# Performance work log

Hardware: AMD Instinct MI355X
Metric: run time of the kernel (lower is better)

## Reference

```python
import jax, jax.numpy as jnp
import numpy as np

B, T, C, F = 32, 512, 256, 512


def setup_inputs() -> dict:
    key = jax.random.key(0)
    k1, k2, k3 = jax.random.split(key, 3)
    x = jax.random.normal(k1, (B, T, F), dtype=jnp.float32)
    # glorot-uniform-ish learned params
    context = jax.random.normal(k2, (C, F), dtype=jnp.float32) * (1.0 / np.sqrt(F))
    W = jax.random.normal(k3, (2 * F, 1), dtype=jnp.float32) * (1.0 / np.sqrt(2 * F))
    b = jnp.zeros((1,), dtype=jnp.float32)
    return {"x": x, "context": context, "W": W, "b": b}


def reference(x, context, W, b):
    # Original: concat(tile(x)->[B,T,C,F], tile(context)->[B,T,C,F]) @ W[2F,1] + b.
    # Decompose W = [W_x; W_c] so the [B,T,C,2F] tensor is never materialized.
    f = x.shape[-1]
    s_x = x @ W[:f] + b            # [B, T, 1]
    s_c = context @ W[f:]          # [C, 1]
    scores = s_x[:, :, None, :] + s_c[None, None, :, :]  # [B, T, C, 1]
    # Keras Activation('softmax') acts on the LAST axis (size 1) -> all ones;
    # computed literally for faithfulness.
    att = jax.nn.softmax(scores, axis=-1)[..., 0]        # [B, T, C]
    # multiply by expanded_x and sum over time axis (axis=1)
    out = jnp.einsum('btc,btf->bcf', att, x)             # [B, C, F]
    return out
```

## Files before the change

kernel.cpp:

```cpp
#include <hip/hip_runtime.h>


#define BB 32
#define TT 512
#define CC 256
#define FF 512
#define F4 (FF / 4)
#define FC 8

__device__ __forceinline__ void acc4(float4& a, const float4& v) {
    a.x += v.x; a.y += v.y; a.z += v.z; a.w += v.w;
}

__global__ __launch_bounds__(512) void colsum_bcast(const float4* __restrict__ x4,
                                                    float4* __restrict__ out4) {
    __shared__ float4 lds[32][16];

    const int tid = threadIdx.x;
    const int f4l = tid & 15;
    const int g   = tid >> 4;
    const int b   = blockIdx.x >> 3;
    const int fc  = blockIdx.x & 7;

    const float4* xp = x4 + (size_t)b * TT * F4 + fc * 16 + f4l;
    float4 a = make_float4(0.f, 0.f, 0.f, 0.f);
#pragma unroll
    for (int k = 0; k < 16; ++k) {
        float4 v = xp[(size_t)(g + 32 * k) * F4];
        acc4(a, v);
    }
    lds[g][f4l] = a;
    __syncthreads();

    if (tid < 16) {
        float4 s = lds[0][tid];
#pragma unroll
        for (int r = 1; r < 32; ++r) acc4(s, lds[r][tid]);
        lds[0][tid] = s;
    }
    __syncthreads();
    const float4 s = lds[0][f4l];

    float4* op = out4 + (size_t)b * CC * F4 + fc * 16 + f4l;
#pragma unroll
    for (int k = 0; k < 8; ++k) {
        op[(size_t)(g + 32 * k) * F4] = s;
    }
}

extern "C" void kernel_launch(void* const* d_in, const int* in_sizes, int n_in,
                              void* d_out, int out_size, void* d_ws, size_t ws_size,
                              hipStream_t stream) {
    const float* x = (const float*)d_in[0];
    float* out = (float*)d_out;
    (void)d_ws; (void)ws_size;

    colsum_bcast<<<BB * FC, 512, 0, stream>>>((const float4*)x, (float4*)out);
}
```

Baseline: 82.74 us.

## Split column sum into partial-sum and reduce-broadcast kernels for more parallelism

Replaces the single fused kernel (256 blocks, each reducing all 512 timesteps for a 64-feature slice) with two kernels. The first computes per-chunk partial sums over 32-row time chunks across 512 blocks and writes them to workspace. The second reduces the 16 partials and broadcasts the result to the output across 512 blocks. Blocks now read full 2KB rows, so accesses are more contiguous. The cost is a second launch and a small workspace round trip.

```diff
diff --git a/kernel.cpp b/kernel.cpp
--- a/kernel.cpp
+++ b/kernel.cpp
@@ -5,46 +5,67 @@
 #define TT 512
 #define CC 256
 #define FF 512
-#define F4 (FF / 4)
-#define FC 8
+#define F4 128
+#define NCH 16
+#define CG 16
 
 __device__ __forceinline__ void acc4(float4& a, const float4& v) {
     a.x += v.x; a.y += v.y; a.z += v.z; a.w += v.w;
 }
 
-__global__ __launch_bounds__(512) void colsum_bcast(const float4* __restrict__ x4,
-                                                    float4* __restrict__ out4) {
-    __shared__ float4 lds[32][16];
+__global__ __launch_bounds__(256) void colsum_partial(const float4* __restrict__ x4,
+                                                      float4* __restrict__ part4) {
+    __shared__ float4 lds[F4];
+    const int tid = threadIdx.x;
+    const int c4  = tid & 127;
+    const int rp  = tid >> 7;
+    const int b   = blockIdx.x >> 4;
+    const int ch  = blockIdx.x & 15;
 
-    const int tid = threadIdx.x;
-    const int f4l = tid & 15;
-    const int g   = tid >> 4;
-    const int b   = blockIdx.x >> 3;
-    const int fc  = blockIdx.x & 7;
-
-    const float4* xp = x4 + (size_t)b * TT * F4 + fc * 16 + f4l;
+    const float4* xp = x4 + ((size_t)(b * TT + ch * 32 + rp) * F4) + c4;
     float4 a = make_float4(0.f, 0.f, 0.f, 0.f);
 #pragma unroll
     for (int k = 0; k < 16; ++k) {
-        float4 v = xp[(size_t)(g + 32 * k) * F4];
-        acc4(a, v);
+        acc4(a, xp[(size_t)(2 * k) * F4]);
     }
-    lds[g][f4l] = a;
+
+    if (rp == 1) lds[c4] = a;
     __syncthreads();
+    if (rp == 0) {
+        acc4(a, lds[c4]);
+        part4[(size_t)(b * NCH + ch) * F4 + c4] = a;
+    }
+}
 
-    if (tid < 16) {
-        float4 s = lds[0][tid];
+__global__ __launch_bounds__(256) void reduce_bcast(const float4* __restrict__ part4,
+                                                    float4* __restrict__ out4) {
+    __shared__ float4 lds[F4];
+    const int tid = threadIdx.x;
+    const int c4  = tid & 127;
+    const int rp  = tid >> 7;
+    const int b   = blockIdx.x >> 4;
+    const int cg  = blockIdx.x & 15;
+
+    const float4* pp = part4 + (size_t)(b * NCH + rp) * F4 + c4;
+    float4 a = make_float4(0.f, 0.f, 0.f, 0.f);
 #pragma unroll
-        for (int r = 1; r < 32; ++r) acc4(s, lds[r][tid]);
-        lds[0][tid] = s;
+    for (int k = 0; k < 8; ++k) {
+        acc4(a, pp[(size_t)(2 * k) * F4]);
+    }
+
+    if (rp == 1) lds[c4] = a;
+    __syncthreads();
+    if (rp == 0) {
+        acc4(a, lds[c4]);
+        lds[c4] = a;
     }
     __syncthreads();
-    const float4 s = lds[0][f4l];
+    const float4 s = lds[c4];
 
-    float4* op = out4 + (size_t)b * CC * F4 + fc * 16 + f4l;
+    float4* op = out4 + (size_t)(b * CC + cg * 16 + rp) * F4 + c4;
 #pragma unroll
     for (int k = 0; k < 8; ++k) {
-        op[(size_t)(g + 32 * k) * F4] = s;
+        op[(size_t)(2 * k) * F4] = s;
     }
 }
 
@@ -53,7 +74,8 @@
                               hipStream_t stream) {
     const float* x = (const float*)d_in[0];
     float* out = (float*)d_out;
-    (void)d_ws; (void)ws_size;
 
-    colsum_bcast<<<BB * FC, 512, 0, stream>>>((const float4*)x, (float4*)out);
+    float4* part = (float4*)d_ws;
+    colsum_partial<<<BB * NCH, 256, 0, stream>>>((const float4*)x, part);
+    reduce_bcast<<<BB * CG, 256, 0, stream>>>(part, (float4*)out);
 }
```

Measured after the change: 85.88 us. 3.8% more time.
